# Performance work log

Measured on AMD Instinct MI355X. Metric: run time of the kernel, lower is better.

Reference implementation:

```python
import jax, jax.numpy as jnp
import numpy as np
from functools import partial

T_DEC, T_ENC = 64, 256
B, E, D = 32, 256, 512   # batch, audio_encoder_size(=input_size), decoder_hidden_size
N_MEL = 80               # spectral_size == n_mel_channels


def setup_inputs() -> dict:
    key = jax.random.key(0)
    ks = jax.random.split(key, 9)
    s = 0.02
    return {
        "decoder_inputs": jax.random.normal(ks[0], (T_DEC, B, E), jnp.float32),
        "alignment_inputs": jax.random.normal(ks[1], (T_ENC, B, E), jnp.float32),
        "W_att": jax.random.normal(ks[2], (E, D), jnp.float32) * s,      # LinearNorm(D->E, no bias)
        "W_ih": jax.random.normal(ks[3], (3 * D, 2 * E), jnp.float32) * s,  # GRUCell input weights (r,z,n)
        "W_hh": jax.random.normal(ks[4], (3 * D, D), jnp.float32) * s,      # GRUCell hidden weights
        "W_mel": jax.random.normal(ks[5], (N_MEL, D + E), jnp.float32) * s,
        "b_mel": jax.random.normal(ks[6], (N_MEL,), jnp.float32) * s,
        "W_gate": jax.random.normal(ks[7], (1, D + E), jnp.float32) * s,
        "b_gate": jax.random.normal(ks[8], (1,), jnp.float32) * s,
    }


def _decode_loop(decoder_inputs, alignment_inputs, W_att, W_ih, W_hh, W_mel, b_mel, W_gate, b_gate):
    Bd, Dd = decoder_inputs.shape[1], W_hh.shape[1]

    def step(h, dec_in):
        # --- Attention: per-feature softmax over encoder time, collapsed over features ---
        proj = h @ W_att.T                                  # (B, E)
        scores = alignment_inputs * proj[None]              # (T_enc, B, E)
        w = jax.nn.softmax(scores, axis=0)                  # softmax over encoder time
        tw = w.sum(axis=-1)                                 # (T_enc, B): sum of per-feature weights
        ctx = jnp.einsum('tb,tbe->be', tw, alignment_inputs)  # (B, E)
        # --- GRUCell (bias=False) ---
        x = jnp.concatenate([dec_in, ctx], axis=-1)         # (B, 2E)
        gi = x @ W_ih.T                                     # (B, 3D)
        gh = h @ W_hh.T                                     # (B, 3D)
        ir, iz, inn = jnp.split(gi, 3, axis=-1)
        hr, hz, hn = jnp.split(gh, 3, axis=-1)
        r = jax.nn.sigmoid(ir + hr)
        z = jax.nn.sigmoid(iz + hz)
        n = jnp.tanh(inn + r * hn)
        h_new = (1.0 - z) * n + z * h
        h_new = jax.nn.relu(h_new)                          # relu(dropout(h)), dropout=0
        # --- Output heads ---
        dhac = jnp.concatenate([ctx, h_new], axis=-1)       # (B, E+D)
        mel = dhac @ W_mel.T + b_mel                        # (B, N_MEL)
        gate = dhac @ W_gate.T + b_gate                     # (B, 1)
        return h_new, (mel, gate)

    # prepend zero init frame, drop last frame (teacher forcing, T_dec steps)
    init_frame = jnp.zeros((1,) + decoder_inputs.shape[1:], decoder_inputs.dtype)
    seq = jnp.concatenate([init_frame, decoder_inputs[:-1]], axis=0)
    h0 = jnp.zeros((Bd, Dd), decoder_inputs.dtype)
    _, (mels, gates) = jax.lax.scan(step, h0, seq)
    # parse_decoder_outputs
    n_mel = W_mel.shape[0]
    mel_out = mels.transpose(1, 0, 2).reshape(Bd, -1, n_mel).transpose(0, 2, 1)  # (B, n_mel, T_dec)
    gate_out = gates.transpose(1, 0, 2)                                          # (B, T_dec, 1)
    return mel_out, gate_out


def reference(decoder_inputs, alignment_inputs, W_att, W_ih, W_hh, W_mel, b_mel, W_gate, b_gate):
    return _decode_loop(decoder_inputs, alignment_inputs, W_att, W_ih, W_hh,
                        W_mel, b_mel, W_gate, b_gate)
```

## Files before the change

### kernel.cpp

```cpp
#include <hip/hip_runtime.h>
#include <hip/hip_bf16.h>


#define LOG2E 1.4426950408889634f
#define FLAGS_MAGIC 0x13572468u
#define SMEM_BYTES 138752
#define NBLK 162

typedef __attribute__((ext_vector_type(8))) short bf8;
typedef __attribute__((ext_vector_type(4))) float f32x4;
typedef __attribute__((ext_vector_type(4))) unsigned u32x4;
typedef unsigned long long ull;

#define EX2(x) exp2f(x)
#define MFMA16(a, b, c) __builtin_amdgcn_mfma_f32_16x16x32_bf16(a, b, c, 0, 0, 0)

struct Params {
  const float* dec;
  const float* ali;
  const float* watt;
  const float* wih;
  const float* whh;
  const float* wmel;
  const float* bmel;
  const float* wgate;
  const float* bgate;
  float* out;
  unsigned* bar;
  __hip_bfloat16* wihb;
  __hip_bfloat16* whhb;
  __hip_bfloat16* wmelgb;
  __hip_bfloat16* seqb;
  __hip_bfloat16* hbf;
  __hip_bfloat16* ctxb;
  unsigned* wattp;
};

__device__ __forceinline__ bf8 ldfrag(const __hip_bfloat16* p) { return *(const bf8*)p; }
__device__ __forceinline__ float sigm(float x) { return 1.0f / (1.0f + EX2(-x * LOG2E)); }
__device__ __forceinline__ float tanhfast(float x) {
  x = fminf(fmaxf(x, -15.0f), 15.0f);
  float e = EX2(x * (2.0f * LOG2E));
  return (e - 1.0f) / (e + 1.0f);
}
__device__ __forceinline__ float btof(unsigned v) { return __uint_as_float(v << 16); }
__device__ __forceinline__ unsigned short f2bfbits(float x) {
  __hip_bfloat16 h = __float2bfloat16(x);
  return *(unsigned short*)&h;
}
__device__ __forceinline__ unsigned sysld32(const unsigned* p) {
  return __hip_atomic_load(p, __ATOMIC_RELAXED, __HIP_MEMORY_SCOPE_SYSTEM);
}
__device__ __forceinline__ ull sysld64(const ull* p) {
  return __hip_atomic_load(p, __ATOMIC_RELAXED, __HIP_MEMORY_SCOPE_SYSTEM);
}
__device__ __forceinline__ void sysst32(unsigned* p, unsigned v) {
  __hip_atomic_store(p, v, __ATOMIC_RELAXED, __HIP_MEMORY_SCOPE_SYSTEM);
}
__device__ __forceinline__ void sysst64(ull* p, ull v) {
  __hip_atomic_store(p, v, __ATOMIC_RELAXED, __HIP_MEMORY_SCOPE_SYSTEM);
}
__device__ __forceinline__ void sysld16x4(u32x4* d0, u32x4* d1, u32x4* d2, u32x4* d3,
                                          const void* p0, const void* p1,
                                          const void* p2, const void* p3) {
  u32x4 a, b, c, d;
  asm volatile(
      "global_load_dwordx4 %0, %4, off sc0 sc1\n\t"
      "global_load_dwordx4 %1, %5, off sc0 sc1\n\t"
      "global_load_dwordx4 %2, %6, off sc0 sc1\n\t"
      "global_load_dwordx4 %3, %7, off sc0 sc1\n\t"
      "s_waitcnt vmcnt(0)"
      : "=&v"(a), "=&v"(b), "=&v"(c), "=&v"(d)
      : "v"(p0), "v"(p1), "v"(p2), "v"(p3)
      : "memory");
  *d0 = a; *d1 = b; *d2 = c; *d3 = d;
}
__device__ __forceinline__ void waitge(unsigned* w, unsigned tgt) {
  while (sysld32(w) < tgt) __builtin_amdgcn_s_sleep(1);
}

__device__ __forceinline__ void p0bar(unsigned* bar) {
  __syncthreads();
  if (threadIdx.x == 0) {
    __builtin_amdgcn_fence(__ATOMIC_RELEASE, "agent");
    __hip_atomic_fetch_add(bar + 16, 1u, __ATOMIC_RELAXED, __HIP_MEMORY_SCOPE_SYSTEM);
    while (sysld32(bar + 16) < (unsigned)NBLK) __builtin_amdgcn_s_sleep(1);
    __builtin_amdgcn_fence(__ATOMIC_ACQUIRE, "agent");
  }
  __syncthreads();
}

__device__ __forceinline__ void p0a_worker(const Params& p, int wid) {
  for (int i = wid; i < 2252800; i += 17408) {
    if (i < 786432) {
      p.wihb[i] = __float2bfloat16(p.wih[i]);
    } else if (i < 1572864) {
      int j = i - 786432;
      p.whhb[j] = __float2bfloat16(p.whh[j]);
    } else if (i < 2097152) {
      int j = i - 1572864;
      int s = j >> 13;
      p.seqb[j] = (s == 0) ? __float2bfloat16(0.0f) : __float2bfloat16(p.dec[j - 8192]);
    } else if (i < 2170880) {
      int j = i - 2097152;
      int r = j / 768, c = j - r * 768;
      float v = (r < 80) ? p.wmel[j] : ((r == 80) ? p.wgate[c] : 0.0f);
      p.wmelgb[j] = __float2bfloat16(v);
    } else if (i < 2236416) {
      int j = i - 2170880;
      int kp = j >> 8, e = j & 255;
      unsigned lo = f2bfbits(p.watt[e * 512 + 2 * kp]);
      unsigned hi = f2bfbits(p.watt[e * 512 + 2 * kp + 1]);
      p.wattp[j] = lo | (hi << 16);
    } else {
      int j = i - 2236416;
      p.hbf[j] = __float2bfloat16(0.0f);
    }
  }
}

__device__ __forceinline__ void stage_h_frag(__hip_bfloat16* hA,
                                             const __hip_bfloat16* hsrc, int tid) {
  const int lm = tid & 15, lq = (tid >> 4) & 3, wq = tid >> 6;
  const int dst_in = (lq * 16 + lm) * 8;
  const int i0 = wq, i1 = 8 + wq, i2 = 16 + wq, i3 = 24 + wq;
  auto soff = [&](int idx) {
    return ((idx >> 4) * 16 + lm) * 512 + (idx & 15) * 32 + lq * 8;
  };
  u32x4 a, b, c, d;
  sysld16x4(&a, &b, &c, &d, hsrc + soff(i0), hsrc + soff(i1), hsrc + soff(i2),
            hsrc + soff(i3));
  u32x4* dst = (u32x4*)hA;
  dst[(i0 * 512 + dst_in) >> 3] = a;
  dst[(i1 * 512 + dst_in) >> 3] = b;
  dst[(i2 * 512 + dst_in) >> 3] = c;
  dst[(i3 * 512 + dst_in) >> 3] = d;
}
__device__ __forceinline__ void stage_c4(__hip_bfloat16* cA,
                                         const __hip_bfloat16* csrc, int tid) {
  const int lm = tid & 15, lq = (tid >> 4) & 3, wq = tid >> 6;
  const int dst_in = (lq * 16 + lm) * 8;
  u32x4* dst = (u32x4*)cA;
  auto soff = [&](int idx) {
    int mt = idx >> 5, kt = idx & 31;
    int bb = mt * 16 + lm;
    int k = kt * 32 + lq * 8;
    return ((k >> 8) * 32 + bb) * 256 + (k & 255);
  };
#pragma unroll
  for (int r = 0; r < 2; ++r) {
    const int i0 = (4 * r + 0) * 8 + wq, i1 = (4 * r + 1) * 8 + wq;
    const int i2 = (4 * r + 2) * 8 + wq, i3 = (4 * r + 3) * 8 + wq;
    u32x4 a, b, c, d;
    sysld16x4(&a, &b, &c, &d, csrc + soff(i0), csrc + soff(i1), csrc + soff(i2),
              csrc + soff(i3));
    dst[(i0 * 512 + dst_in) >> 3] = a;
    dst[(i1 * 512 + dst_in) >> 3] = b;
    dst[(i2 * 512 + dst_in) >> 3] = c;
    dst[(i3 * 512 + dst_in) >> 3] = d;
  }
}

__global__ void __launch_bounds__(512, 1) rdec_kernel(Params p) {
  const int tid = threadIdx.x;
  const int bid = blockIdx.x;
  extern __shared__ char smem[];
  unsigned* hdone = p.bar + 32;
  unsigned* ctxdone = p.bar + 544;
  unsigned* meldone = p.bar + 2592;

  if (bid == 0) {
    for (int i = 1 + tid; i < 2624; i += 512) sysst32(p.bar + i, 0u);
    __syncthreads();
    if (tid == 0) sysst32(p.bar, FLAGS_MAGIC);
  }

  if (bid < 128) {
    const int b = bid >> 2, q4 = bid & 3, hb = q4 * 32 + b;
    unsigned short* alds = (unsigned short*)smem;
    float* fb = (float*)(smem + 133120);
    float* shh = fb;
    float* p2l = fb + 512;
    float* rzl = fb + 576;
    float* tw = fb + 640;
    float* cp = fb + 896;

    const int el = tid >> 3, kq = tid & 7;
    const int f = tid & 255, th = tid >> 8;

    for (int i = tid; i < 65536; i += 512) {
      int t = i >> 8, ee = i & 255;
      alds[ee * 260 + t] = f2bfbits(p.ali[t * 8192 + b * 256 + ee]);
    }
    if (tid == 0) {
      while (sysld32(p.bar) != FLAGS_MAGIC) __builtin_amdgcn_s_sleep(1);
    }
    p0bar(p.bar);
    unsigned wr[32];
#pragma unroll
    for (int i = 0; i < 32; ++i) wr[i] = p.wattp[(i * 8 + kq) * 256 + q4 * 64 + el];

    for (int s = 0; s < 64; ++s) {
      if (tid < 32) waitge(hdone + tid * 16, (unsigned)s);
      else if (tid < 34) waitge(meldone + (tid - 32) * 16, (s >= 4) ? (unsigned)(s - 3) : 0u);
      __syncthreads();
      if (tid < 128) {
        ull w = sysld64((const ull*)(p.hbf + (s & 3) * 16384 + b * 512) + tid);
        shh[tid * 4 + 0] = btof((unsigned)(w & 0xffff));
        shh[tid * 4 + 1] = btof((unsigned)((w >> 16) & 0xffff));
        shh[tid * 4 + 2] = btof((unsigned)((w >> 32) & 0xffff));
        shh[tid * 4 + 3] = btof((unsigned)((w >> 48) & 0xffff));
      }
      __syncthreads();
      {
        const float2* h2 = (const float2*)shh;
        float a0 = 0.f, a1 = 0.f;
#pragma unroll
        for (int i = 0; i < 32; i += 2) {
          unsigned w0 = wr[i], w1 = wr[i + 1];
          float2 h0 = h2[i * 8 + kq], h1 = h2[(i + 1) * 8 + kq];
          a0 = fmaf(__uint_as_float(w0 << 16), h0.x, a0);
          a0 = fmaf(__uint_as_float(w0 & 0xffff0000u), h0.y, a0);
          a1 = fmaf(__uint_as_float(w1 << 16), h1.x, a1);
          a1 = fmaf(__uint_as_float(w1 & 0xffff0000u), h1.y, a1);
        }
        float pr = a0 + a1;
        pr += __shfl_xor(pr, 1);
        pr += __shfl_xor(pr, 2);
        pr += __shfl_xor(pr, 4);
        const float pp = pr * LOG2E;
        const unsigned short* ap = alds + (q4 * 64 + el) * 260 + kq * 32;
        float z0 = 0.f, z1 = 0.f;
#pragma unroll
        for (int j = 0; j < 8; ++j) {
          ushort4 v = *(const ushort4*)(ap + j * 4);
          z0 += EX2(btof(v.x) * pp) + EX2(btof(v.y) * pp);
          z1 += EX2(btof(v.z) * pp) + EX2(btof(v.w) * pp);
        }
        float zz = z0 + z1;
        zz += __shfl_xor(zz, 1);
        zz += __shfl_xor(zz, 2);
        zz += __shfl_xor(zz, 4);
        if (kq == 0) {
          p2l[el] = pp;
          rzl[el] = 1.0f / zz;
        }
      }
      __syncthreads();
      {
        float t0 = 0.f, t1 = 0.f, t2 = 0.f, t3 = 0.f;
#pragma unroll
        for (int j = 0; j < 8; ++j) {
          const int e2 = kq * 8 + j;
          ushort4 v = *(const ushort4*)(alds + (q4 * 64 + e2) * 260 + el * 4);
          const float ppj = p2l[e2], rr = rzl[e2];
          t0 = fmaf(EX2(btof(v.x) * ppj), rr, t0);
          t1 = fmaf(EX2(btof(v.y) * ppj), rr, t1);
          t2 = fmaf(EX2(btof(v.z) * ppj), rr, t2);
          t3 = fmaf(EX2(btof(v.w) * ppj), rr, t3);
        }
        t0 += __shfl_xor(t0, 1); t0 += __shfl_xor(t0, 2); t0 += __shfl_xor(t0, 4);
        t1 += __shfl_xor(t1, 1); t1 += __shfl_xor(t1, 2); t1 += __shfl_xor(t1, 4);
        t2 += __shfl_xor(t2, 1); t2 += __shfl_xor(t2, 2); t2 += __shfl_xor(t2, 4);
        t3 += __shfl_xor(t3, 1); t3 += __shfl_xor(t3, 2); t3 += __shfl_xor(t3, 4);
        if (kq == 0) *(float4*)(tw + el * 4) = make_float4(t0, t1, t2, t3);
      }
      __syncthreads();
      {
        const unsigned short* ap = alds + f * 260 + th * 128;
        const float4* twv = (const float4*)(tw + th * 128);
        float c0 = 0.f, c1 = 0.f;
#pragma unroll 4
        for (int j = 0; j < 32; ++j) {
          ushort4 v = *(const ushort4*)(ap + j * 4);
          float4 t4 = twv[j];
          c0 += t4.x * btof(v.x) + t4.y * btof(v.y);
          c1 += t4.z * btof(v.z) + t4.w * btof(v.w);
        }
        cp[th * 256 + f] = c0 + c1;
      }
      __syncthreads();
      if (tid < 128) {
        float2 ca = ((const float2*)cp)[tid];
        float2 cb = ((const float2*)(cp + 256))[tid];
        float cv0 = ca.x + cb.x, cv1 = ca.y + cb.y;
        unsigned u = (unsigned)f2bfbits(cv0) | ((unsigned)f2bfbits(cv1) << 16);
        sysst32((unsigned*)(p.ctxb + ((s & 3) * 128 + hb) * 256) + tid, u);
      }
      __syncthreads();
      if (tid == 0) sysst32(ctxdone + hb * 16, (unsigned)(s + 1));
    }
  } else if (bid < 160) {
    const int dt = bid - 128;
    const int wv = tid >> 6;
    const bool act = wv < 6;
    const int l = tid & 63, lm = l & 15, lq = l >> 4;
    const int g = wv % 3, mt = wv / 3;
    const int am = mt * 16 + lm;
    const int brow = g * 512 + dt * 16 + lm;
    __hip_bfloat16* hA = (__hip_bfloat16*)smem;
    __hip_bfloat16* cA = (__hip_bfloat16*)(smem + 32768);
    float* pw = (float*)(smem + 98304);
    unsigned short* h16 = (unsigned short*)(smem + 107008);
    p0a_worker(p, (bid - 128) * 512 + tid);
    if (tid == 0) {
      while (sysld32(p.bar) != FLAGS_MAGIC) __builtin_amdgcn_s_sleep(1);
    }
    p0bar(p.bar);
    bf8 WH[16], WD[8], WC[8];
    if (act) {
#pragma unroll
      for (int kt = 0; kt < 16; ++kt) WH[kt] = ldfrag(p.whhb + brow * 512 + kt * 32 + lq * 8);
#pragma unroll
      for (int kt = 0; kt < 8; ++kt) WD[kt] = ldfrag(p.wihb + brow * 512 + kt * 32 + lq * 8);
#pragma unroll
      for (int kt = 0; kt < 8; ++kt) WC[kt] = ldfrag(p.wihb + brow * 512 + 256 + kt * 32 + lq * 8);
    }
    for (int s = 0; s < 64; ++s) {
      if (tid < 32) waitge(hdone + tid * 16, (unsigned)s);
      else if (tid < 34) waitge(meldone + (tid - 32) * 16, (s >= 4) ? (unsigned)(s - 3) : 0u);
      __syncthreads();
      stage_h_frag(hA, p.hbf + (s & 3) * 16384, tid);
      __syncthreads();
      f32x4 acc = {0.f, 0.f, 0.f, 0.f};
      f32x4 gi = {0.f, 0.f, 0.f, 0.f};
      if (act) {
#pragma unroll
        for (int kt = 0; kt < 16; ++kt) {
          bf8 a = ldfrag(hA + (mt * 16 + kt) * 512 + l * 8);
          acc = MFMA16(a, WH[kt], acc);
        }
        const __hip_bfloat16* seqp = p.seqb + s * 8192;
#pragma unroll
        for (int kt = 0; kt < 8; ++kt) {
          bf8 a = ldfrag(seqp + am * 256 + kt * 32 + lq * 8);
          gi = MFMA16(a, WD[kt], gi);
        }
      }
      if (tid < 128) waitge(ctxdone + tid * 16, (unsigned)(s + 1));
      __syncthreads();
      stage_c4(cA, p.ctxb + (s & 3) * 32768, tid);
      __syncthreads();
      if (act) {
#pragma unroll
        for (int kt = 0; kt < 32; ++kt) {
          bf8 a = ldfrag(cA + (mt * 32 + kt) * 512 + l * 8);
          gi = MFMA16(a, WC[kt & 7], gi);
        }
        if (g < 2) {
#pragma unroll
          for (int r = 0; r < 4; ++r) pw[(wv * 16 + lq * 4 + r) * 17 + lm] = acc[r] + gi[r];
        } else {
#pragma unroll
          for (int r = 0; r < 4; ++r) pw[(wv * 16 + lq * 4 + r) * 17 + lm] = acc[r];
#pragma unroll
          for (int r = 0; r < 4; ++r) pw[((6 + mt) * 16 + lq * 4 + r) * 17 + lm] = gi[r];
        }
      }
      __syncthreads();
      {
        const int bb = tid >> 4, dl = tid & 15;
        const int mtb = bb >> 4, bl = bb & 15;
        float rg = sigm(pw[((mtb * 3 + 0) * 16 + bl) * 17 + dl]);
        float zg = sigm(pw[((mtb * 3 + 1) * 16 + bl) * 17 + dl]);
        float hn = pw[((mtb * 3 + 2) * 16 + bl) * 17 + dl];
        float inn = pw[((6 + mtb) * 16 + bl) * 17 + dl];
        float nn = tanhfast(fmaf(rg, hn, inn));
        const int d = dt * 16 + dl;
        float ho = btof(((unsigned short*)hA)[((bb >> 4) * 16 + (d >> 5)) * 512 +
                                              (((d >> 3) & 3) * 16 + (bb & 15)) * 8 +
                                              (d & 7)]);
        float hnew = fmaxf(0.0f, fmaf(zg, ho - nn, nn));
        h16[bb * 16 + dl] = f2bfbits(hnew);
      }
      __syncthreads();
      if (tid < 256) {
        const int bb2 = tid >> 3, dp = tid & 7;
        unsigned v = (unsigned)h16[bb2 * 16 + dp * 2] |
                     ((unsigned)h16[bb2 * 16 + dp * 2 + 1] << 16);
        sysst32((unsigned*)(p.hbf + ((s + 1) & 3) * 16384) + bb2 * 256 + dt * 8 + dp, v);
      }
      __syncthreads();
      if (tid == 0) sysst32(hdone + dt * 16, (unsigned)(s + 1));
    }
  } else {
    const int mt = bid - 160;
    const int wv = tid >> 6;
    const bool act = wv < 6;
    const int l = tid & 63, lm = l & 15, lq = l >> 4;
    const int nt = wv;
    const int bn = nt * 16 + lm;
    __hip_bfloat16* hA = (__hip_bfloat16*)smem;
    __hip_bfloat16* cA = (__hip_bfloat16*)(smem + 32768);
    p0a_worker(p, (bid - 128) * 512 + tid);
    if (tid == 0) {
      while (sysld32(p.bar) != FLAGS_MAGIC) __builtin_amdgcn_s_sleep(1);
    }
    p0bar(p.bar);
    bf8 WMC[8], WMH[16];
    float bias = 0.f;
    if (act) {
#pragma unroll
      for (int kt = 0; kt < 8; ++kt) WMC[kt] = ldfrag(p.wmelgb + bn * 768 + kt * 32 + lq * 8);
#pragma unroll
      for (int kt = 0; kt < 16; ++kt)
        WMH[kt] = ldfrag(p.wmelgb + bn * 768 + 256 + kt * 32 + lq * 8);
      bias = (bn < 80) ? p.bmel[bn] : ((bn == 80) ? p.bgate[0] : 0.f);
    }
    for (int tau = 0; tau < 64; ++tau) {
      if (tid < 32) waitge(hdone + tid * 16, (unsigned)(tau + 1));
      else if (tid >= 64 && tid < 192) waitge(ctxdone + (tid - 64) * 16, (unsigned)(tau + 1));
      __syncthreads();
      stage_h_frag(hA, p.hbf + ((tau + 1) & 3) * 16384, tid);
      stage_c4(cA, p.ctxb + (tau & 3) * 32768, tid);
      __syncthreads();
      if (act) {
        f32x4 acc = {0.f, 0.f, 0.f, 0.f};
#pragma unroll
        for (int kt = 0; kt < 48; ++kt) {
          bf8 a = (kt < 32) ? ldfrag(cA + (mt * 32 + kt) * 512 + l * 8)
                            : ldfrag(hA + (mt * 16 + (kt - 32)) * 512 + l * 8);
          bf8 bb2 = (kt < 32) ? WMC[kt & 7] : WMH[kt - 32];
          acc = MFMA16(a, bb2, acc);
        }
#pragma unroll
        for (int r = 0; r < 4; ++r) {
          int bb = mt * 16 + lq * 4 + r;
          float v = acc[r] + bias;
          if (bn < 80)
            p.out[bb * 5120 + bn * 64 + tau] = v;
          else if (bn == 80)
            p.out[163840 + bb * 64 + tau] = v;
        }
      }
      __syncthreads();
      if (tid == 0) sysst32(meldone + mt * 16, (unsigned)(tau + 1));
    }
  }
}

extern "C" void kernel_launch(void* const* d_in, const int* in_sizes, int n_in,
                              void* d_out, int out_size, void* d_ws, size_t ws_size,
                              hipStream_t stream) {
  Params P;
  P.dec = (const float*)d_in[0];
  P.ali = (const float*)d_in[1];
  P.watt = (const float*)d_in[2];
  P.wih = (const float*)d_in[3];
  P.whh = (const float*)d_in[4];
  P.wmel = (const float*)d_in[5];
  P.bmel = (const float*)d_in[6];
  P.wgate = (const float*)d_in[7];
  P.bgate = (const float*)d_in[8];
  P.out = (float*)d_out;

  char* w = (char*)d_ws;
  size_t o = 0;
  auto nxt = [&](size_t b) {
    char* r = w + o;
    o += (b + 255) & ~(size_t)255;
    return r;
  };
  P.bar = (unsigned*)nxt(16384);
  P.wihb = (__hip_bfloat16*)nxt(1536 * 512 * 2);
  P.whhb = (__hip_bfloat16*)nxt(1536 * 512 * 2);
  P.wmelgb = (__hip_bfloat16*)nxt(96 * 768 * 2);
  P.seqb = (__hip_bfloat16*)nxt(64 * 32 * 256 * 2);
  P.hbf = (__hip_bfloat16*)nxt(4 * 32 * 512 * 2);
  P.ctxb = (__hip_bfloat16*)nxt(4 * 128 * 256 * 2);
  P.wattp = (unsigned*)nxt(256 * 256 * 4);

  (void)hipFuncSetAttribute((const void*)rdec_kernel,
                            hipFuncAttributeMaxDynamicSharedMemorySize, SMEM_BYTES);

  void* args[] = {&P};
  hipError_t err = hipLaunchCooperativeKernel((void*)rdec_kernel, dim3(NBLK), dim3(512),
                                              args, SMEM_BYTES, stream);
  if (err != hipSuccess) {
    rdec_kernel<<<dim3(NBLK), dim3(512), SMEM_BYTES, stream>>>(P);
  }
}
```

Baseline: 833.3 us.

## Use per-step h/ctx buffers to drop mel backpressure and system-scope loads

Replaces the 4-slot ring buffers for hidden state and context with a full per-timestep history (65 and 64 slots). This lets the code drop the meldone flag waits that held producers back and switch consumer loads from system-scope sc0/sc1 atomics to ordinary vector loads. The attention-projection thread mapping is also reshuffled so the reduction runs across lanes 8/16/32, which changes the wattp and LDS access patterns. In exchange it uses more workspace memory and depends on plain loads never seeing stale cached lines, which holds only because each address is written once before it is read.

Measured after the change: 809.6 us. 2.9% less time.

```diff
diff --git a/kernel.cpp b/kernel.cpp
--- a/kernel.cpp
+++ b/kernel.cpp
@@ -51,29 +51,8 @@
 __device__ __forceinline__ unsigned sysld32(const unsigned* p) {
   return __hip_atomic_load(p, __ATOMIC_RELAXED, __HIP_MEMORY_SCOPE_SYSTEM);
 }
-__device__ __forceinline__ ull sysld64(const ull* p) {
-  return __hip_atomic_load(p, __ATOMIC_RELAXED, __HIP_MEMORY_SCOPE_SYSTEM);
-}
 __device__ __forceinline__ void sysst32(unsigned* p, unsigned v) {
   __hip_atomic_store(p, v, __ATOMIC_RELAXED, __HIP_MEMORY_SCOPE_SYSTEM);
-}
-__device__ __forceinline__ void sysst64(ull* p, ull v) {
-  __hip_atomic_store(p, v, __ATOMIC_RELAXED, __HIP_MEMORY_SCOPE_SYSTEM);
-}
-__device__ __forceinline__ void sysld16x4(u32x4* d0, u32x4* d1, u32x4* d2, u32x4* d3,
-                                          const void* p0, const void* p1,
-                                          const void* p2, const void* p3) {
-  u32x4 a, b, c, d;
-  asm volatile(
-      "global_load_dwordx4 %0, %4, off sc0 sc1\n\t"
-      "global_load_dwordx4 %1, %5, off sc0 sc1\n\t"
-      "global_load_dwordx4 %2, %6, off sc0 sc1\n\t"
-      "global_load_dwordx4 %3, %7, off sc0 sc1\n\t"
-      "s_waitcnt vmcnt(0)"
-      : "=&v"(a), "=&v"(b), "=&v"(c), "=&v"(d)
-      : "v"(p0), "v"(p1), "v"(p2), "v"(p3)
-      : "memory");
-  *d0 = a; *d1 = b; *d2 = c; *d3 = d;
 }
 __device__ __forceinline__ void waitge(unsigned* w, unsigned tgt) {
   while (sysld32(w) < tgt) __builtin_amdgcn_s_sleep(1);
@@ -127,9 +106,10 @@
   auto soff = [&](int idx) {
     return ((idx >> 4) * 16 + lm) * 512 + (idx & 15) * 32 + lq * 8;
   };
-  u32x4 a, b, c, d;
-  sysld16x4(&a, &b, &c, &d, hsrc + soff(i0), hsrc + soff(i1), hsrc + soff(i2),
-            hsrc + soff(i3));
+  u32x4 a = *(const u32x4*)(hsrc + soff(i0));
+  u32x4 b = *(const u32x4*)(hsrc + soff(i1));
+  u32x4 c = *(const u32x4*)(hsrc + soff(i2));
+  u32x4 d = *(const u32x4*)(hsrc + soff(i3));
   u32x4* dst = (u32x4*)hA;
   dst[(i0 * 512 + dst_in) >> 3] = a;
   dst[(i1 * 512 + dst_in) >> 3] = b;
@@ -148,16 +128,10 @@
     return ((k >> 8) * 32 + bb) * 256 + (k & 255);
   };
 #pragma unroll
-  for (int r = 0; r < 2; ++r) {
-    const int i0 = (4 * r + 0) * 8 + wq, i1 = (4 * r + 1) * 8 + wq;
-    const int i2 = (4 * r + 2) * 8 + wq, i3 = (4 * r + 3) * 8 + wq;
-    u32x4 a, b, c, d;
-    sysld16x4(&a, &b, &c, &d, csrc + soff(i0), csrc + soff(i1), csrc + soff(i2),
-              csrc + soff(i3));
-    dst[(i0 * 512 + dst_in) >> 3] = a;
-    dst[(i1 * 512 + dst_in) >> 3] = b;
-    dst[(i2 * 512 + dst_in) >> 3] = c;
-    dst[(i3 * 512 + dst_in) >> 3] = d;
+  for (int r = 0; r < 8; ++r) {
+    const int idx = r * 8 + wq;
+    u32x4 v = *(const u32x4*)(csrc + soff(idx));
+    dst[(idx * 512 + dst_in) >> 3] = v;
   }
 }
 
@@ -167,7 +141,6 @@
   extern __shared__ char smem[];
   unsigned* hdone = p.bar + 32;
   unsigned* ctxdone = p.bar + 544;
-  unsigned* meldone = p.bar + 2592;
 
   if (bid == 0) {
     for (int i = 1 + tid; i < 2624; i += 512) sysst32(p.bar + i, 0u);
@@ -185,7 +158,8 @@
     float* tw = fb + 640;
     float* cp = fb + 896;
 
-    const int el = tid >> 3, kq = tid & 7;
+    const int el = (tid & 7) | ((tid >> 6) << 3);
+    const int kq = (tid >> 3) & 7;
     const int f = tid & 255, th = tid >> 8;
 
     for (int i = tid; i < 65536; i += 512) {
@@ -202,10 +176,9 @@
 
     for (int s = 0; s < 64; ++s) {
       if (tid < 32) waitge(hdone + tid * 16, (unsigned)s);
-      else if (tid < 34) waitge(meldone + (tid - 32) * 16, (s >= 4) ? (unsigned)(s - 3) : 0u);
       __syncthreads();
       if (tid < 128) {
-        ull w = sysld64((const ull*)(p.hbf + (s & 3) * 16384 + b * 512) + tid);
+        ull w = ((const ull*)(p.hbf + s * 16384 + b * 512))[tid];
         shh[tid * 4 + 0] = btof((unsigned)(w & 0xffff));
         shh[tid * 4 + 1] = btof((unsigned)((w >> 16) & 0xffff));
         shh[tid * 4 + 2] = btof((unsigned)((w >> 32) & 0xffff));
@@ -225,9 +198,9 @@
           a1 = fmaf(__uint_as_float(w1 & 0xffff0000u), h1.y, a1);
         }
         float pr = a0 + a1;
-        pr += __shfl_xor(pr, 1);
-        pr += __shfl_xor(pr, 2);
-        pr += __shfl_xor(pr, 4);
+        pr += __shfl_xor(pr, 8);
+        pr += __shfl_xor(pr, 16);
+        pr += __shfl_xor(pr, 32);
         const float pp = pr * LOG2E;
         const unsigned short* ap = alds + (q4 * 64 + el) * 260 + kq * 32;
         float z0 = 0.f, z1 = 0.f;
@@ -238,9 +211,9 @@
           z1 += EX2(btof(v.z) * pp) + EX2(btof(v.w) * pp);
         }
         float zz = z0 + z1;
-        zz += __shfl_xor(zz, 1);
-        zz += __shfl_xor(zz, 2);
-        zz += __shfl_xor(zz, 4);
+        zz += __shfl_xor(zz, 8);
+        zz += __shfl_xor(zz, 16);
+        zz += __shfl_xor(zz, 32);
         if (kq == 0) {
           p2l[el] = pp;
           rzl[el] = 1.0f / zz;
@@ -259,10 +232,10 @@
           t2 = fmaf(EX2(btof(v.z) * ppj), rr, t2);
           t3 = fmaf(EX2(btof(v.w) * ppj), rr, t3);
         }
-        t0 += __shfl_xor(t0, 1); t0 += __shfl_xor(t0, 2); t0 += __shfl_xor(t0, 4);
-        t1 += __shfl_xor(t1, 1); t1 += __shfl_xor(t1, 2); t1 += __shfl_xor(t1, 4);
-        t2 += __shfl_xor(t2, 1); t2 += __shfl_xor(t2, 2); t2 += __shfl_xor(t2, 4);
-        t3 += __shfl_xor(t3, 1); t3 += __shfl_xor(t3, 2); t3 += __shfl_xor(t3, 4);
+        t0 += __shfl_xor(t0, 8); t0 += __shfl_xor(t0, 16); t0 += __shfl_xor(t0, 32);
+        t1 += __shfl_xor(t1, 8); t1 += __shfl_xor(t1, 16); t1 += __shfl_xor(t1, 32);
+        t2 += __shfl_xor(t2, 8); t2 += __shfl_xor(t2, 16); t2 += __shfl_xor(t2, 32);
+        t3 += __shfl_xor(t3, 8); t3 += __shfl_xor(t3, 16); t3 += __shfl_xor(t3, 32);
         if (kq == 0) *(float4*)(tw + el * 4) = make_float4(t0, t1, t2, t3);
       }
       __syncthreads();
@@ -285,7 +258,7 @@
         float2 cb = ((const float2*)(cp + 256))[tid];
         float cv0 = ca.x + cb.x, cv1 = ca.y + cb.y;
         unsigned u = (unsigned)f2bfbits(cv0) | ((unsigned)f2bfbits(cv1) << 16);
-        sysst32((unsigned*)(p.ctxb + ((s & 3) * 128 + hb) * 256) + tid, u);
+        sysst32((unsigned*)(p.ctxb + (s * 128 + hb) * 256) + tid, u);
       }
       __syncthreads();
       if (tid == 0) sysst32(ctxdone + hb * 16, (unsigned)(s + 1));
@@ -318,9 +291,8 @@
     }
     for (int s = 0; s < 64; ++s) {
       if (tid < 32) waitge(hdone + tid * 16, (unsigned)s);
-      else if (tid < 34) waitge(meldone + (tid - 32) * 16, (s >= 4) ? (unsigned)(s - 3) : 0u);
-      __syncthreads();
-      stage_h_frag(hA, p.hbf + (s & 3) * 16384, tid);
+      __syncthreads();
+      stage_h_frag(hA, p.hbf + s * 16384, tid);
       __syncthreads();
       f32x4 acc = {0.f, 0.f, 0.f, 0.f};
       f32x4 gi = {0.f, 0.f, 0.f, 0.f};
@@ -339,7 +311,7 @@
       }
       if (tid < 128) waitge(ctxdone + tid * 16, (unsigned)(s + 1));
       __syncthreads();
-      stage_c4(cA, p.ctxb + (s & 3) * 32768, tid);
+      stage_c4(cA, p.ctxb + s * 32768, tid);
       __syncthreads();
       if (act) {
 #pragma unroll
@@ -378,7 +350,7 @@
         const int bb2 = tid >> 3, dp = tid & 7;
         unsigned v = (unsigned)h16[bb2 * 16 + dp * 2] |
                      ((unsigned)h16[bb2 * 16 + dp * 2 + 1] << 16);
-        sysst32((unsigned*)(p.hbf + ((s + 1) & 3) * 16384) + bb2 * 256 + dt * 8 + dp, v);
+        sysst32((unsigned*)(p.hbf + (s + 1) * 16384) + bb2 * 256 + dt * 8 + dp, v);
       }
       __syncthreads();
       if (tid == 0) sysst32(hdone + dt * 16, (unsigned)(s + 1));
@@ -411,8 +383,8 @@
       if (tid < 32) waitge(hdone + tid * 16, (unsigned)(tau + 1));
       else if (tid >= 64 && tid < 192) waitge(ctxdone + (tid - 64) * 16, (unsigned)(tau + 1));
       __syncthreads();
-      stage_h_frag(hA, p.hbf + ((tau + 1) & 3) * 16384, tid);
-      stage_c4(cA, p.ctxb + (tau & 3) * 32768, tid);
+      stage_h_frag(hA, p.hbf + (tau + 1) * 16384, tid);
+      stage_c4(cA, p.ctxb + tau * 32768, tid);
       __syncthreads();
       if (act) {
         f32x4 acc = {0.f, 0.f, 0.f, 0.f};
@@ -434,7 +406,6 @@
         }
       }
       __syncthreads();
-      if (tid == 0) sysst32(meldone + mt * 16, (unsigned)(tau + 1));
     }
   }
 }
@@ -466,8 +437,8 @@
   P.whhb = (__hip_bfloat16*)nxt(1536 * 512 * 2);
   P.wmelgb = (__hip_bfloat16*)nxt(96 * 768 * 2);
   P.seqb = (__hip_bfloat16*)nxt(64 * 32 * 256 * 2);
-  P.hbf = (__hip_bfloat16*)nxt(4 * 32 * 512 * 2);
-  P.ctxb = (__hip_bfloat16*)nxt(4 * 128 * 256 * 2);
+  P.hbf = (__hip_bfloat16*)nxt(65 * 32 * 512 * 2);
+  P.ctxb = (__hip_bfloat16*)nxt(64 * 128 * 256 * 2);
   P.wattp = (unsigned*)nxt(256 * 256 * 4);
 
   (void)hipFuncSetAttribute((const void*)rdec_kernel,
```
